# Kernel tuning notes

Measured on AMD Instinct MI355X. Metric: run time of the kernel, lower is better.

Reference implementation:

```python
import jax, jax.numpy as jnp
import numpy as np

D_MODEL = 1024
NUM_HEADS = 16
THRESHOLD = 0.1


def setup_inputs() -> dict:
    key = jax.random.key(0)
    ks = jax.random.split(key, 12)
    B, L, D, C = 2, 2048, D_MODEL, 8
    s = 1.0 / np.sqrt(D)
    inp = {
        "q_x": jax.random.normal(ks[0], (B, L, D), jnp.float32),
        "k_x": jax.random.normal(ks[1], (B, L, D), jnp.float32),
        "v_x": jax.random.normal(ks[2], (B, L, D), jnp.float32),
        "energy_coeffs": jax.random.normal(ks[3], (B, L, C), jnp.float32),
        "Wq": jax.random.normal(ks[4], (D, D), jnp.float32) * s,
        "bq": jnp.zeros((D,), jnp.float32),
        "Wk": jax.random.normal(ks[5], (D, D), jnp.float32) * s,
        "bk": jnp.zeros((D,), jnp.float32),
        "Wv": jax.random.normal(ks[6], (D, D), jnp.float32) * s,
        "bv": jnp.zeros((D,), jnp.float32),
        "Wo": jax.random.normal(ks[7], (D, D), jnp.float32) * s,
        "bo": jnp.zeros((D,), jnp.float32),
    }
    return inp


def reference(q_x, k_x, v_x, energy_coeffs, Wq, bq, Wk, bk, Wv, bv, Wo, bo):
    B, L, D = q_x.shape
    H = NUM_HEADS
    Dh = D // H
    # projections -> (B, H, L, Dh)
    def proj(x, W, b):
        y = x @ W + b
        return y.reshape(B, -1, H, Dh).transpose(0, 2, 1, 3)
    Q = proj(q_x, Wq, bq)
    K = proj(k_x, Wk, bk)
    V = proj(v_x, Wv, bv)
    scores = jnp.einsum("bhqd,bhkd->bhqk", Q, K) / np.sqrt(Dh).astype(np.float32)
    attn = jax.nn.softmax(scores, axis=-1)
    attn = jnp.nan_to_num(attn, nan=0.0)
    # post-softmax energy gate over key positions
    energy = jnp.abs(energy_coeffs).mean(axis=-1)  # (B, Lk)
    gate = jax.nn.sigmoid((energy - THRESHOLD) * 10.0)[:, None, None, :]
    attn = attn * gate
    out = jnp.einsum("bhqk,bhkd->bhqd", attn, V)
    out = out.transpose(0, 2, 1, 3).reshape(B, L, D)
    return out @ Wo + bo
```

## Files before the change

kernel.cpp:

```cpp
#include <hip/hip_runtime.h>

typedef __attribute__((ext_vector_type(8))) short bf16x8;
typedef __attribute__((ext_vector_type(8))) unsigned short u16x8;
typedef __attribute__((ext_vector_type(4))) float f32x4;
typedef __attribute__((ext_vector_type(4))) unsigned int u32x4;

#define DEVI static __device__ __forceinline__

typedef const __attribute__((address_space(1))) void cglobal_void;
typedef __attribute__((address_space(3))) void lds_void;
#define GLD16(gp, lp) __builtin_amdgcn_global_load_lds((cglobal_void*)(gp), (lds_void*)(lp), 16, 0, 0)

DEVI unsigned short f2bf(float x) {
  unsigned int u = __builtin_bit_cast(unsigned int, x);
  u += 0x7fffu + ((u >> 16) & 1u);
  return (unsigned short)(u >> 16);
}
DEVI unsigned int cvtpk_bf16(float lo, float hi) {
  unsigned int r;
  asm("v_cvt_pk_bf16_f32 %0, %1, %2" : "=v"(r) : "v"(lo), "v"(hi));
  return r;
}
DEVI float fast_exp2(float x) {
  float r;
  asm("v_exp_f32 %0, %1" : "=v"(r) : "v"(x));
  return r;
}

__global__ void k_gate(const float* __restrict__ E, float* __restrict__ gate) {
  int i = blockIdx.x * 256 + threadIdx.x;
  const float4* e = reinterpret_cast<const float4*>(E);
  float4 a = e[i * 2], b = e[i * 2 + 1];
  float s = fabsf(a.x) + fabsf(a.y) + fabsf(a.z) + fabsf(a.w)
          + fabsf(b.x) + fabsf(b.y) + fabsf(b.z) + fabsf(b.w);
  float en = s * 0.125f;
  gate[i] = 1.0f / (1.0f + __expf(-10.0f * (en - 0.1f)));
}

__global__ void k_pack_plain3(const float* __restrict__ X0, const float* __restrict__ X1,
                              const float* __restrict__ X2, unsigned short* __restrict__ Xp) {
  const float* X = (blockIdx.y == 0) ? X0 : (blockIdx.y == 1) ? X1 : X2;
  int t = blockIdx.x * 256 + threadIdx.x;
  int idx = t << 3;
  const float4* src = reinterpret_cast<const float4*>(X + idx);
  float4 a = src[0], b = src[1];
  float xs[8] = {a.x, a.y, a.z, a.w, b.x, b.y, b.z, b.w};
  u16x8 hi;
#pragma unroll
  for (int j = 0; j < 8; ++j) hi[j] = f2bf(xs[j]);
  *reinterpret_cast<u16x8*>(Xp + (size_t)blockIdx.y * 4194304 + idx) = hi;
}

__global__ void k_pack_wT4(const float* __restrict__ W0, const float* __restrict__ W1,
                           const float* __restrict__ W2, const float* __restrict__ W3,
                           unsigned short* __restrict__ Wt) {
  const float* W = (blockIdx.z == 0) ? W0 : (blockIdx.z == 1) ? W1
                 : (blockIdx.z == 2) ? W2 : W3;
  unsigned short* D = Wt + (size_t)blockIdx.z * 1048576;
  __shared__ float tile[32][33];
  int tx = threadIdx.x & 31, ty = threadIdx.x >> 5;
  int kb = blockIdx.x * 32, nb = blockIdx.y * 32;
#pragma unroll
  for (int i = 0; i < 4; ++i)
    tile[ty + 8 * i][tx] = W[(size_t)(kb + ty + 8 * i) * 1024 + nb + tx];
  __syncthreads();
#pragma unroll
  for (int i = 0; i < 4; ++i) {
    int n = nb + ty + 8 * i;
    int k = kb + tx;
    D[(size_t)n * 1024 + k] = f2bf(tile[tx][ty + 8 * i]);
  }
}

template <int NT>
DEVI void gemm_tile(const unsigned short* __restrict__ A,
                    const unsigned short* __restrict__ Bt,
                    unsigned short* sA0, unsigned short* sB0,
                    int m0, int n0, int tid, f32x4 acc[4][4]) {
  const int lane = tid & 63;
  const int l15 = lane & 15, l4 = lane >> 4;
  const int wave = tid >> 6;
  const int wr = wave >> 1, wc = wave & 1;
  const int wofs = (tid & 192) * 16;

  auto stage = [&](int buf, int k0) {
    unsigned short* dA = sA0 + buf * 8192;
    unsigned short* dB = sB0 + buf * 8192;
#pragma unroll
    for (int i = 0; i < 4; ++i) {
      int id = i * 256 + tid;
      int r = id >> 3, c = id & 7;
      GLD16(A + (size_t)(m0 + r) * 1024 + k0 + ((c ^ (r & 7)) << 3), (char*)dA + i * 4096 + wofs);
    }
#pragma unroll
    for (int i = 0; i < 4; ++i) {
      int id = i * 256 + tid;
      int r = id >> 3, c = id & 7;
      GLD16(Bt + (size_t)(n0 + r) * 1024 + k0 + ((c ^ (r & 7)) << 3), (char*)dB + i * 4096 + wofs);
    }
  };

  stage(0, 0);
  int cur = 0;
  for (int t = 0; t < NT; ++t) {
    __syncthreads();
    if (t + 1 < NT) stage(cur ^ 1, (t + 1) * 64);
    const unsigned short* cA = sA0 + cur * 8192;
    const unsigned short* cB = sB0 + cur * 8192;
#pragma unroll
    for (int kc = 0; kc < 2; ++kc) {
      bf16x8 af[4], bfr[4];
#pragma unroll
      for (int f = 0; f < 4; ++f) {
        int r = wr * 64 + f * 16 + l15;
        af[f] = *reinterpret_cast<const bf16x8*>(
            reinterpret_cast<const char*>(cA) + r * 128 + (((kc * 4 + l4) ^ (r & 7)) * 16));
      }
#pragma unroll
      for (int f = 0; f < 4; ++f) {
        int r = wc * 64 + f * 16 + l15;
        bfr[f] = *reinterpret_cast<const bf16x8*>(
            reinterpret_cast<const char*>(cB) + r * 128 + (((kc * 4 + l4) ^ (r & 7)) * 16));
      }
      __builtin_amdgcn_s_setprio(1);
#pragma unroll
      for (int fm = 0; fm < 4; ++fm)
#pragma unroll
        for (int fn = 0; fn < 4; ++fn)
          acc[fm][fn] = __builtin_amdgcn_mfma_f32_16x16x32_bf16(af[fm], bfr[fn], acc[fm][fn], 0, 0, 0);
      __builtin_amdgcn_s_setprio(0);
    }
    cur ^= 1;
  }
}

__global__ __launch_bounds__(256) void k_gemm_qkv(const unsigned short* __restrict__ Xqkv,
                                                  const unsigned short* __restrict__ WhQ,
                                                  const unsigned short* __restrict__ WhK,
                                                  const unsigned short* __restrict__ WhV,
                                                  const float* __restrict__ bq,
                                                  const float* __restrict__ bk,
                                                  const float* __restrict__ bv,
                                                  const float* __restrict__ gate,
                                                  unsigned short* __restrict__ Qp,
                                                  unsigned short* __restrict__ Kp,
                                                  unsigned short* __restrict__ Vt) {
  __shared__ unsigned short sA[2][128 * 64];
  __shared__ unsigned short sB[2][128 * 64];
  const int tid = threadIdx.x;
  const int lane = tid & 63, wave = tid >> 6;
  const int l15 = lane & 15, l4 = lane >> 4;
  const int wr = wave >> 1, wc = wave & 1;
  const int m0 = blockIdx.x * 128, n0 = blockIdx.y * 128;
  const int region = m0 >> 12;
  const unsigned short* Wm = (region == 0) ? WhQ : (region == 1) ? WhK : WhV;
  const float* bias = (region == 0) ? bq : (region == 1) ? bk : bv;

  const f32x4 zero4 = {0.f, 0.f, 0.f, 0.f};
  f32x4 acc[4][4];
#pragma unroll
  for (int i = 0; i < 4; ++i)
#pragma unroll
    for (int j = 0; j < 4; ++j) acc[i][j] = zero4;

  gemm_tile<16>(Wm, Xqkv, &sA[0][0], &sB[0][0], n0, m0, tid, acc);

  if (region < 2) {
    unsigned short* Out = (region == 0) ? Qp : Kp;
    const float scale = (region == 0) ? 0.18033688011112042f : 1.0f;
#pragma unroll
    for (int fw = 0; fw < 4; ++fw) {
      int nb = n0 + wr * 64 + fw * 16 + l4 * 4;
      int h = nb >> 6, d0 = nb & 63;
      float4 bv4 = *reinterpret_cast<const float4*>(bias + nb);
#pragma unroll
      for (int fx = 0; fx < 4; ++fx) {
        int rowm = (m0 + wc * 64 + fx * 16 + l15) & 4095;
        int b = rowm >> 11, l = rowm & 2047;
        float v0 = (acc[fw][fx][0] + bv4.x) * scale;
        float v1 = (acc[fw][fx][1] + bv4.y) * scale;
        float v2 = (acc[fw][fx][2] + bv4.z) * scale;
        float v3 = (acc[fw][fx][3] + bv4.w) * scale;
        uint2 wv;
        wv.x = cvtpk_bf16(v0, v1);
        wv.y = cvtpk_bf16(v2, v3);
        *reinterpret_cast<uint2*>(Out + (((size_t)(b * 16 + h) * 2048 + l) << 6) + d0) = wv;
      }
    }
  } else {
#pragma unroll
    for (int fw = 0; fw < 4; ++fw) {
      int nb = n0 + wr * 64 + fw * 16 + l4 * 4;
      int h = nb >> 6, d0 = nb & 63;
      float4 bv4 = *reinterpret_cast<const float4*>(bias + nb);
#pragma unroll
      for (int fx = 0; fx < 4; ++fx) {
        int rowm = (m0 + wc * 64 + fx * 16 + l15) & 4095;
        int b = rowm >> 11, l = rowm & 2047;
        float g = gate[rowm];
        float vj[4] = {(acc[fw][fx][0] + bv4.x) * g, (acc[fw][fx][1] + bv4.y) * g,
                       (acc[fw][fx][2] + bv4.z) * g, (acc[fw][fx][3] + bv4.w) * g};
#pragma unroll
        for (int j = 0; j < 4; ++j)
          Vt[((size_t)(b * 16 + h) * 64 + d0 + j) * 2048 + l] = f2bf(vj[j]);
      }
    }
  }
}

__global__ __launch_bounds__(256) void k_gemm_f32(const unsigned short* __restrict__ A,
                                                  const unsigned short* __restrict__ Bt,
                                                  const float* __restrict__ bias,
                                                  float* __restrict__ C) {
  __shared__ unsigned short sA[2][128 * 64];
  __shared__ unsigned short sB[2][128 * 64];
  const int tid = threadIdx.x;
  const int lane = tid & 63, wave = tid >> 6;
  const int l15 = lane & 15, l4 = lane >> 4;
  const int wr = wave >> 1, wc = wave & 1;
  const int m0 = blockIdx.x * 128, n0 = blockIdx.y * 128;

  const f32x4 zero4 = {0.f, 0.f, 0.f, 0.f};
  f32x4 acc[4][4];
#pragma unroll
  for (int i = 0; i < 4; ++i)
#pragma unroll
    for (int j = 0; j < 4; ++j) acc[i][j] = zero4;

  gemm_tile<16>(Bt, A, &sA[0][0], &sB[0][0], n0, m0, tid, acc);

#pragma unroll
  for (int fw = 0; fw < 4; ++fw) {
    int col0 = n0 + wr * 64 + fw * 16 + l4 * 4;
    float4 bv4 = *reinterpret_cast<const float4*>(bias + col0);
#pragma unroll
    for (int fx = 0; fx < 4; ++fx) {
      int row = m0 + wc * 64 + fx * 16 + l15;
      float4 o;
      o.x = acc[fw][fx][0] + bv4.x;
      o.y = acc[fw][fx][1] + bv4.y;
      o.z = acc[fw][fx][2] + bv4.z;
      o.w = acc[fw][fx][3] + bv4.w;
      *reinterpret_cast<float4*>(C + (size_t)row * 1024 + col0) = o;
    }
  }
}

__global__ __launch_bounds__(256) void k_flash(const unsigned short* __restrict__ Qp,
                                               const unsigned short* __restrict__ Kp,
                                               const unsigned short* __restrict__ Vt,
                                               unsigned short* __restrict__ O) {
  __shared__ unsigned short sK[3][64 * 64];
  __shared__ unsigned short sV[3][64 * 64];
  const int tid = threadIdx.x;
  const int lane = tid & 63, wave = tid >> 6;
  const int l15 = lane & 15, l4 = lane >> 4;
  const int bh = blockIdx.x;
  const int q0 = blockIdx.y * 128;
  const int b = bh >> 4, h = bh & 15;
  const size_t hBase = (size_t)bh * 2048 * 64;
  const int wofs = (tid & 192) * 16;

  bf16x8 qf[2][2];
#pragma unroll
  for (int fq = 0; fq < 2; ++fq) {
    int qrow = q0 + wave * 32 + fq * 16 + l15;
#pragma unroll
    for (int kc = 0; kc < 2; ++kc)
      qf[fq][kc] = *reinterpret_cast<const bf16x8*>(Qp + hBase + (size_t)qrow * 64 + kc * 32 + l4 * 8);
  }

  const short one_bf = 0x3F80;
  const bf16x8 ones = {one_bf, one_bf, one_bf, one_bf, one_bf, one_bf, one_bf, one_bf};

  const f32x4 zero4 = {0.f, 0.f, 0.f, 0.f};
  f32x4 accO[2][4];
  f32x4 accL[2];
#pragma unroll
  for (int fq = 0; fq < 2; ++fq) {
    accL[fq] = zero4;
#pragma unroll
    for (int fd = 0; fd < 4; ++fd) accO[fq][fd] = zero4;
  }

  auto stage = [&](int buf, int kv0) {
#pragma unroll
    for (int i = 0; i < 2; ++i) {
      int id = i * 256 + tid;
      int r = id >> 3, c = id & 7;
      int sc = (c ^ (r & 7)) << 3;
      int kr = (r & 32) | ((r & 12) << 1) | ((r & 16) >> 2) | (r & 3);
      GLD16(Kp + hBase + (size_t)(kv0 + kr) * 64 + sc, (char*)sK[buf] + i * 4096 + wofs);
      GLD16(Vt + hBase + (size_t)r * 2048 + kv0 + sc, (char*)sV[buf] + i * 4096 + wofs);
    }
  };

  auto tile = [&](int t, int cb, int sb, bool last, bool dostage) {
    if (last) { asm volatile("s_waitcnt vmcnt(0)" ::: "memory"); }
    else      { asm volatile("s_waitcnt vmcnt(4)" ::: "memory"); }
    __builtin_amdgcn_sched_barrier(0);
    __builtin_amdgcn_s_barrier();
    __builtin_amdgcn_sched_barrier(0);

    f32x4 s[4][2];
#pragma unroll
    for (int fk = 0; fk < 4; ++fk)
#pragma unroll
      for (int fq = 0; fq < 2; ++fq) s[fk][fq] = zero4;
#pragma unroll
    for (int kc = 0; kc < 2; ++kc) {
      bf16x8 kf[4];
#pragma unroll
      for (int fk = 0; fk < 4; ++fk) {
        int r = fk * 16 + l15;
        kf[fk] = *reinterpret_cast<const bf16x8*>(
            reinterpret_cast<const char*>(sK[cb]) + r * 128 + (((kc * 4 + l4) ^ (r & 7)) * 16));
      }
      __builtin_amdgcn_s_setprio(1);
#pragma unroll
      for (int fk = 0; fk < 4; ++fk)
#pragma unroll
        for (int fq = 0; fq < 2; ++fq)
          s[fk][fq] = __builtin_amdgcn_mfma_f32_16x16x32_bf16(kf[fk], qf[fq][kc], s[fk][fq], 0, 0, 0);
      __builtin_amdgcn_s_setprio(0);
    }

    if (dostage) stage(sb, (t + 2) * 64);

    u32x4 pfa[2][2];
#pragma unroll
    for (int fq = 0; fq < 2; ++fq) {
      float p[4][4];
#pragma unroll
      for (int fk = 0; fk < 4; ++fk)
#pragma unroll
        for (int j = 0; j < 4; ++j) p[fk][j] = fast_exp2(s[fk][fq][j]);
      pfa[fq][0].x = cvtpk_bf16(p[0][0], p[0][1]);
      pfa[fq][0].y = cvtpk_bf16(p[0][2], p[0][3]);
      pfa[fq][0].z = cvtpk_bf16(p[1][0], p[1][1]);
      pfa[fq][0].w = cvtpk_bf16(p[1][2], p[1][3]);
      pfa[fq][1].x = cvtpk_bf16(p[2][0], p[2][1]);
      pfa[fq][1].y = cvtpk_bf16(p[2][2], p[2][3]);
      pfa[fq][1].z = cvtpk_bf16(p[3][0], p[3][1]);
      pfa[fq][1].w = cvtpk_bf16(p[3][2], p[3][3]);
    }

#pragma unroll
    for (int kc = 0; kc < 2; ++kc) {
      bf16x8 vf[4];
#pragma unroll
      for (int fd = 0; fd < 4; ++fd) {
        int r = fd * 16 + l15;
        vf[fd] = *reinterpret_cast<const bf16x8*>(
            reinterpret_cast<const char*>(sV[cb]) + r * 128 + (((kc * 4 + l4) ^ (r & 7)) * 16));
      }
      __builtin_amdgcn_s_setprio(1);
#pragma unroll
      for (int fq = 0; fq < 2; ++fq) {
        bf16x8 pf = __builtin_bit_cast(bf16x8, pfa[fq][kc]);
#pragma unroll
        for (int fd = 0; fd < 4; ++fd)
          accO[fq][fd] = __builtin_amdgcn_mfma_f32_16x16x32_bf16(pf, vf[fd], accO[fq][fd], 0, 0, 0);
        accL[fq] = __builtin_amdgcn_mfma_f32_16x16x32_bf16(pf, ones, accL[fq], 0, 0, 0);
      }
      __builtin_amdgcn_s_setprio(0);
    }
  };

  stage(0, 0);
  stage(1, 64);

  for (int base = 0; base < 30; base += 3) {
    tile(base + 0, 0, 2, false, true);
    tile(base + 1, 1, 0, false, true);
    tile(base + 2, 2, 1, false, true);
  }
  tile(30, 0, 2, false, false);
  tile(31, 1, 0, true, false);

#pragma unroll
  for (int fq = 0; fq < 2; ++fq)
#pragma unroll
    for (int j = 0; j < 4; ++j) {
      float li = 1.0f / accL[fq][j];
      int qw = q0 + wave * 32 + fq * 16 + l4 * 4 + j;
#pragma unroll
      for (int fd = 0; fd < 4; ++fd) {
        int col = h * 64 + fd * 16 + l15;
        O[(size_t)(b * 2048 + qw) * 1024 + col] = f2bf(accO[fq][fd][j] * li);
      }
    }
}

extern "C" void kernel_launch(void* const* d_in, const int* in_sizes, int n_in,
                              void* d_out, int out_size, void* d_ws, size_t ws_size,
                              hipStream_t stream) {
  const float* q_x = (const float*)d_in[0];
  const float* k_x = (const float*)d_in[1];
  const float* v_x = (const float*)d_in[2];
  const float* E   = (const float*)d_in[3];
  const float* Wq  = (const float*)d_in[4];
  const float* bq  = (const float*)d_in[5];
  const float* Wk  = (const float*)d_in[6];
  const float* bk  = (const float*)d_in[7];
  const float* Wv  = (const float*)d_in[8];
  const float* bv  = (const float*)d_in[9];
  const float* Wo  = (const float*)d_in[10];
  const float* bo  = (const float*)d_in[11];
  float* out = (float*)d_out;

  char* w = (char*)d_ws;
  unsigned short* Wt4  = (unsigned short*)(w + 0);
  unsigned short* Whq  = Wt4;
  unsigned short* Whk  = Wt4 + 1048576;
  unsigned short* Wtv  = Wt4 + 2097152;
  unsigned short* Wto  = Wt4 + 3145728;
  unsigned short* Xqkv = (unsigned short*)(w + 8388608);
  unsigned short* Qp   = (unsigned short*)(w + 33554432);
  unsigned short* Kpp  = (unsigned short*)(w + 41943040);
  unsigned short* Vtp  = (unsigned short*)(w + 50331648);
  unsigned short* Obf  = (unsigned short*)(w + 58720256);
  float*          gate = (float*)(w + 67108864);

  k_gate<<<16, 256, 0, stream>>>(E, gate);

  k_pack_wT4<<<dim3(32, 32, 4), 256, 0, stream>>>(Wq, Wk, Wv, Wo, Wt4);

  k_pack_plain3<<<dim3(2048, 3), 256, 0, stream>>>(q_x, k_x, v_x, Xqkv);

  k_gemm_qkv<<<dim3(96, 8), 256, 0, stream>>>(Xqkv, Whq, Whk, Wtv, bq, bk, bv, gate,
                                              Qp, Kpp, Vtp);

  k_flash<<<dim3(32, 16), 256, 0, stream>>>(Qp, Kpp, Vtp, Obf);

  k_gemm_f32<<<dim3(32, 8), 256, 0, stream>>>(Obf, Wto, bo, out);
}
```

Baseline: 126.8 us.

## Fuse fp32-to-bf16 activation conversion into QKV GEMM operand loading

Removes the separate pack kernel that converted q_x/k_x/v_x to bf16 in workspace, and instead has the QKV GEMM load fp32 activations directly into registers, convert them with packed bf16 instructions, and write them swizzled into LDS. The register load for the next tile is issued before the MFMA loop and the LDS write after it, to overlap global latency with compute. This saves a full write+read of the bf16 activation buffer and one launch. In exchange, each GEMM block reads fp32 (twice the bytes) and re-reads the activations across the 8 N-blocks, and the path uses more registers.

```diff
diff --git a/kernel.cpp b/kernel.cpp
--- a/kernel.cpp
+++ b/kernel.cpp
@@ -35,20 +35,6 @@
           + fabsf(b.x) + fabsf(b.y) + fabsf(b.z) + fabsf(b.w);
   float en = s * 0.125f;
   gate[i] = 1.0f / (1.0f + __expf(-10.0f * (en - 0.1f)));
-}
-
-__global__ void k_pack_plain3(const float* __restrict__ X0, const float* __restrict__ X1,
-                              const float* __restrict__ X2, unsigned short* __restrict__ Xp) {
-  const float* X = (blockIdx.y == 0) ? X0 : (blockIdx.y == 1) ? X1 : X2;
-  int t = blockIdx.x * 256 + threadIdx.x;
-  int idx = t << 3;
-  const float4* src = reinterpret_cast<const float4*>(X + idx);
-  float4 a = src[0], b = src[1];
-  float xs[8] = {a.x, a.y, a.z, a.w, b.x, b.y, b.z, b.w};
-  u16x8 hi;
-#pragma unroll
-  for (int j = 0; j < 8; ++j) hi[j] = f2bf(xs[j]);
-  *reinterpret_cast<u16x8*>(Xp + (size_t)blockIdx.y * 4194304 + idx) = hi;
 }
 
 __global__ void k_pack_wT4(const float* __restrict__ W0, const float* __restrict__ W1,
@@ -134,7 +120,9 @@
   }
 }
 
-__global__ __launch_bounds__(256) void k_gemm_qkv(const unsigned short* __restrict__ Xqkv,
+__global__ __launch_bounds__(256) void k_gemm_qkv(const float* __restrict__ q_x,
+                                                  const float* __restrict__ k_x,
+                                                  const float* __restrict__ v_x,
                                                   const unsigned short* __restrict__ WhQ,
                                                   const unsigned short* __restrict__ WhK,
                                                   const unsigned short* __restrict__ WhV,
@@ -153,8 +141,42 @@
   const int wr = wave >> 1, wc = wave & 1;
   const int m0 = blockIdx.x * 128, n0 = blockIdx.y * 128;
   const int region = m0 >> 12;
+  const float* X = (region == 0) ? q_x : (region == 1) ? k_x : v_x;
   const unsigned short* Wm = (region == 0) ? WhQ : (region == 1) ? WhK : WhV;
   const float* bias = (region == 0) ? bq : (region == 1) ? bk : bv;
+  const int wofs = (tid & 192) * 16;
+  const int xr = tid >> 1;
+  const int xc = (tid & 1) * 32;
+  const size_t xrow = (size_t)((m0 & 4095) + xr) * 1024;
+
+  auto stageA = [&](int buf, int k0) {
+    unsigned short* dA = &sA[buf][0];
+#pragma unroll
+    for (int i = 0; i < 4; ++i) {
+      int id = i * 256 + tid;
+      int r = id >> 3, c = id & 7;
+      GLD16(Wm + (size_t)(n0 + r) * 1024 + k0 + ((c ^ (r & 7)) << 3), (char*)dA + i * 4096 + wofs);
+    }
+  };
+  float4 xb[8];
+  auto loadB = [&](int k0) {
+    const float4* s4 = reinterpret_cast<const float4*>(X + xrow + k0 + xc);
+#pragma unroll
+    for (int i = 0; i < 8; ++i) xb[i] = s4[i];
+  };
+  auto writeB = [&](int buf) {
+    char* base = reinterpret_cast<char*>(&sB[buf][0]) + xr * 128;
+#pragma unroll
+    for (int c4 = 0; c4 < 4; ++c4) {
+      int c = (tid & 1) * 4 + c4;
+      u32x4 wv;
+      wv.x = cvtpk_bf16(xb[c4 * 2].x, xb[c4 * 2].y);
+      wv.y = cvtpk_bf16(xb[c4 * 2].z, xb[c4 * 2].w);
+      wv.z = cvtpk_bf16(xb[c4 * 2 + 1].x, xb[c4 * 2 + 1].y);
+      wv.w = cvtpk_bf16(xb[c4 * 2 + 1].z, xb[c4 * 2 + 1].w);
+      *reinterpret_cast<u32x4*>(base + ((c ^ (xr & 7)) * 16)) = wv;
+    }
+  };
 
   const f32x4 zero4 = {0.f, 0.f, 0.f, 0.f};
   f32x4 acc[4][4];
@@ -163,7 +185,41 @@
 #pragma unroll
     for (int j = 0; j < 4; ++j) acc[i][j] = zero4;
 
-  gemm_tile<16>(Wm, Xqkv, &sA[0][0], &sB[0][0], n0, m0, tid, acc);
+  loadB(0);
+  stageA(0, 0);
+  writeB(0);
+  int cur = 0;
+  for (int t = 0; t < 16; ++t) {
+    __syncthreads();
+    if (t + 1 < 16) { stageA(cur ^ 1, (t + 1) * 64); loadB((t + 1) * 64); }
+    const unsigned short* cA = &sA[cur][0];
+    const unsigned short* cB = &sB[cur][0];
+#pragma unroll
+    for (int kc = 0; kc < 2; ++kc) {
+      bf16x8 af[4], bfr[4];
+#pragma unroll
+      for (int f = 0; f < 4; ++f) {
+        int r = wr * 64 + f * 16 + l15;
+        af[f] = *reinterpret_cast<const bf16x8*>(
+            reinterpret_cast<const char*>(cA) + r * 128 + (((kc * 4 + l4) ^ (r & 7)) * 16));
+      }
+#pragma unroll
+      for (int f = 0; f < 4; ++f) {
+        int r = wc * 64 + f * 16 + l15;
+        bfr[f] = *reinterpret_cast<const bf16x8*>(
+            reinterpret_cast<const char*>(cB) + r * 128 + (((kc * 4 + l4) ^ (r & 7)) * 16));
+      }
+      __builtin_amdgcn_s_setprio(1);
+#pragma unroll
+      for (int fm = 0; fm < 4; ++fm)
+#pragma unroll
+        for (int fn = 0; fn < 4; ++fn)
+          acc[fm][fn] = __builtin_amdgcn_mfma_f32_16x16x32_bf16(af[fm], bfr[fn], acc[fm][fn], 0, 0, 0);
+      __builtin_amdgcn_s_setprio(0);
+    }
+    if (t + 1 < 16) writeB(cur ^ 1);
+    cur ^= 1;
+  }
 
   if (region < 2) {
     unsigned short* Out = (region == 0) ? Qp : Kp;
@@ -415,21 +471,18 @@
   unsigned short* Whk  = Wt4 + 1048576;
   unsigned short* Wtv  = Wt4 + 2097152;
   unsigned short* Wto  = Wt4 + 3145728;
-  unsigned short* Xqkv = (unsigned short*)(w + 8388608);
-  unsigned short* Qp   = (unsigned short*)(w + 33554432);
-  unsigned short* Kpp  = (unsigned short*)(w + 41943040);
-  unsigned short* Vtp  = (unsigned short*)(w + 50331648);
-  unsigned short* Obf  = (unsigned short*)(w + 58720256);
-  float*          gate = (float*)(w + 67108864);
+  unsigned short* Qp   = (unsigned short*)(w + 8388608);
+  unsigned short* Kpp  = (unsigned short*)(w + 16777216);
+  unsigned short* Vtp  = (unsigned short*)(w + 25165824);
+  unsigned short* Obf  = (unsigned short*)(w + 33554432);
+  float*          gate = (float*)(w + 41943040);
 
   k_gate<<<16, 256, 0, stream>>>(E, gate);
 
   k_pack_wT4<<<dim3(32, 32, 4), 256, 0, stream>>>(Wq, Wk, Wv, Wo, Wt4);
 
-  k_pack_plain3<<<dim3(2048, 3), 256, 0, stream>>>(q_x, k_x, v_x, Xqkv);
-
-  k_gemm_qkv<<<dim3(96, 8), 256, 0, stream>>>(Xqkv, Whq, Whk, Wtv, bq, bk, bv, gate,
-                                              Qp, Kpp, Vtp);
+  k_gemm_qkv<<<dim3(96, 8), 256, 0, stream>>>(q_x, k_x, v_x, Whq, Whk, Wtv,
+                                              bq, bk, bv, gate, Qp, Kpp, Vtp);
 
   k_flash<<<dim3(32, 16), 256, 0, stream>>>(Qp, Kpp, Vtp, Obf);
 
```

Measured after the change: 142.6 us. 12.5% more time.

## Switch GEMM mainloop to triple-buffered K=32 stages with explicit vmcnt waits

Applied to the files above, without the earlier changes.

Replaces the double-buffered K=64 GEMM tile loop with a three-stage ring of K=32 LDS buffers. Loads are issued two steps ahead, and an explicit s_waitcnt vmcnt plus a raw s_barrier replace __syncthreads. The LDS swizzle is adapted to 64-byte rows. The aim is to keep more global loads in flight and cut barrier overhead, at the cost of twice as many barriers per K and a hand-tuned wait count that must match the number of loads issued.

```diff
diff --git a/kernel.cpp b/kernel.cpp
--- a/kernel.cpp
+++ b/kernel.cpp
@@ -72,65 +72,70 @@
   }
 }
 
-template <int NT>
-DEVI void gemm_tile(const unsigned short* __restrict__ A,
-                    const unsigned short* __restrict__ Bt,
-                    unsigned short* sA0, unsigned short* sB0,
-                    int m0, int n0, int tid, f32x4 acc[4][4]) {
+DEVI void gemm_tile3(const unsigned short* __restrict__ A,
+                     const unsigned short* __restrict__ Bt,
+                     unsigned short* sA0, unsigned short* sB0,
+                     int m0, int n0, int tid, f32x4 acc[4][4]) {
   const int lane = tid & 63;
   const int l15 = lane & 15, l4 = lane >> 4;
   const int wave = tid >> 6;
   const int wr = wave >> 1, wc = wave & 1;
   const int wofs = (tid & 192) * 16;
+  const int cq = (l4 ^ ((l15 >> 1) & 3)) << 4;
 
   auto stage = [&](int buf, int k0) {
-    unsigned short* dA = sA0 + buf * 8192;
-    unsigned short* dB = sB0 + buf * 8192;
-#pragma unroll
-    for (int i = 0; i < 4; ++i) {
+    unsigned short* dA = sA0 + buf * 4096;
+    unsigned short* dB = sB0 + buf * 4096;
+#pragma unroll
+    for (int i = 0; i < 2; ++i) {
       int id = i * 256 + tid;
-      int r = id >> 3, c = id & 7;
-      GLD16(A + (size_t)(m0 + r) * 1024 + k0 + ((c ^ (r & 7)) << 3), (char*)dA + i * 4096 + wofs);
-    }
-#pragma unroll
-    for (int i = 0; i < 4; ++i) {
+      int r = id >> 2, c = id & 3;
+      int sc = (c ^ ((r >> 1) & 3)) << 3;
+      GLD16(A + (size_t)(m0 + r) * 1024 + k0 + sc, (char*)dA + i * 4096 + wofs);
+    }
+#pragma unroll
+    for (int i = 0; i < 2; ++i) {
       int id = i * 256 + tid;
-      int r = id >> 3, c = id & 7;
-      GLD16(Bt + (size_t)(n0 + r) * 1024 + k0 + ((c ^ (r & 7)) << 3), (char*)dB + i * 4096 + wofs);
+      int r = id >> 2, c = id & 3;
+      int sc = (c ^ ((r >> 1) & 3)) << 3;
+      GLD16(Bt + (size_t)(n0 + r) * 1024 + k0 + sc, (char*)dB + i * 4096 + wofs);
     }
   };
 
   stage(0, 0);
-  int cur = 0;
-  for (int t = 0; t < NT; ++t) {
-    __syncthreads();
-    if (t + 1 < NT) stage(cur ^ 1, (t + 1) * 64);
-    const unsigned short* cA = sA0 + cur * 8192;
-    const unsigned short* cB = sB0 + cur * 8192;
-#pragma unroll
-    for (int kc = 0; kc < 2; ++kc) {
-      bf16x8 af[4], bfr[4];
-#pragma unroll
-      for (int f = 0; f < 4; ++f) {
-        int r = wr * 64 + f * 16 + l15;
-        af[f] = *reinterpret_cast<const bf16x8*>(
-            reinterpret_cast<const char*>(cA) + r * 128 + (((kc * 4 + l4) ^ (r & 7)) * 16));
-      }
-#pragma unroll
-      for (int f = 0; f < 4; ++f) {
-        int r = wc * 64 + f * 16 + l15;
-        bfr[f] = *reinterpret_cast<const bf16x8*>(
-            reinterpret_cast<const char*>(cB) + r * 128 + (((kc * 4 + l4) ^ (r & 7)) * 16));
-      }
-      __builtin_amdgcn_s_setprio(1);
-#pragma unroll
-      for (int fm = 0; fm < 4; ++fm)
-#pragma unroll
-        for (int fn = 0; fn < 4; ++fn)
-          acc[fm][fn] = __builtin_amdgcn_mfma_f32_16x16x32_bf16(af[fm], bfr[fn], acc[fm][fn], 0, 0, 0);
-      __builtin_amdgcn_s_setprio(0);
-    }
-    cur ^= 1;
+  stage(1, 32);
+
+  for (int t = 0; t < 32; ++t) {
+    const int cb = t % 3;
+    if (t < 31) asm volatile("s_waitcnt vmcnt(4)" ::: "memory");
+    else        asm volatile("s_waitcnt vmcnt(0)" ::: "memory");
+    __builtin_amdgcn_sched_barrier(0);
+    __builtin_amdgcn_s_barrier();
+    __builtin_amdgcn_sched_barrier(0);
+
+    const unsigned short* cA = sA0 + cb * 4096;
+    const unsigned short* cB = sB0 + cb * 4096;
+    bf16x8 af[4], bfr[4];
+#pragma unroll
+    for (int f = 0; f < 4; ++f) {
+      int r = wr * 64 + f * 16 + l15;
+      af[f] = *reinterpret_cast<const bf16x8*>(reinterpret_cast<const char*>(cA) + r * 64 + cq);
+    }
+#pragma unroll
+    for (int f = 0; f < 4; ++f) {
+      int r = wc * 64 + f * 16 + l15;
+      bfr[f] = *reinterpret_cast<const bf16x8*>(reinterpret_cast<const char*>(cB) + r * 64 + cq);
+    }
+
+    if (t + 2 < 32) stage((t + 2) % 3, (t + 2) * 32);
+
+    __builtin_amdgcn_s_setprio(1);
+#pragma unroll
+    for (int fm = 0; fm < 4; ++fm)
+#pragma unroll
+      for (int fn = 0; fn < 4; ++fn)
+        acc[fm][fn] = __builtin_amdgcn_mfma_f32_16x16x32_bf16(af[fm], bfr[fn], acc[fm][fn], 0, 0, 0);
+    __builtin_amdgcn_s_setprio(0);
   }
 }
 
@@ -145,8 +150,8 @@
                                                   unsigned short* __restrict__ Qp,
                                                   unsigned short* __restrict__ Kp,
                                                   unsigned short* __restrict__ Vt) {
-  __shared__ unsigned short sA[2][128 * 64];
-  __shared__ unsigned short sB[2][128 * 64];
+  __shared__ unsigned short sA[3][128 * 32];
+  __shared__ unsigned short sB[3][128 * 32];
   const int tid = threadIdx.x;
   const int lane = tid & 63, wave = tid >> 6;
   const int l15 = lane & 15, l4 = lane >> 4;
@@ -163,7 +168,7 @@
 #pragma unroll
     for (int j = 0; j < 4; ++j) acc[i][j] = zero4;
 
-  gemm_tile<16>(Wm, Xqkv, &sA[0][0], &sB[0][0], n0, m0, tid, acc);
+  gemm_tile3(Wm, Xqkv, &sA[0][0], &sB[0][0], n0, m0, tid, acc);
 
   if (region < 2) {
     unsigned short* Out = (region == 0) ? Qp : Kp;
@@ -212,8 +217,8 @@
                                                   const unsigned short* __restrict__ Bt,
                                                   const float* __restrict__ bias,
                                                   float* __restrict__ C) {
-  __shared__ unsigned short sA[2][128 * 64];
-  __shared__ unsigned short sB[2][128 * 64];
+  __shared__ unsigned short sA[3][128 * 32];
+  __shared__ unsigned short sB[3][128 * 32];
   const int tid = threadIdx.x;
   const int lane = tid & 63, wave = tid >> 6;
   const int l15 = lane & 15, l4 = lane >> 4;
@@ -227,7 +232,7 @@
 #pragma unroll
     for (int j = 0; j < 4; ++j) acc[i][j] = zero4;
 
-  gemm_tile<16>(Bt, A, &sA[0][0], &sB[0][0], n0, m0, tid, acc);
+  gemm_tile3(Bt, A, &sA[0][0], &sB[0][0], n0, m0, tid, acc);
 
 #pragma unroll
   for (int fw = 0; fw < 4; ++fw) {
```

After: 124.0 us. 2.2% less time.
